# Optimization experiments

Hardware: AMD Instinct MI355X
Metric: run time of the kernel (lower is better)

Reference implementation:

```python
import jax, jax.numpy as jnp
import numpy as np

HEAD_DIM = 128
NUM_HEADS = 16
NUM_KV_HEADS = 16
ROPE_MAX_POS = 4096
ROPE_BASE = 10000.0


def _rope_tables(seq_len):
    # cos/sin cached tables: [S, D/2]
    inv_freq = 1.0 / (ROPE_BASE ** (jnp.arange(0, HEAD_DIM, 2, dtype=jnp.float32) / HEAD_DIM))
    t = jnp.arange(seq_len, dtype=jnp.float32)
    freqs = jnp.outer(t, inv_freq)
    return jnp.cos(freqs), jnp.sin(freqs)


def _apply_rope(x, cos, sin):
    # x: [B, S, H, D]; cos/sin: [S, D/2] -> broadcast over heads as [S, 1, D/2]
    orig_dtype = x.dtype
    c = cos[:, None, :]
    s = sin[:, None, :]
    xf = x.astype(jnp.float32)
    x_real, x_im = jnp.split(xf, 2, axis=-1)  # half-split (not interleaved) RoPE
    x_real_e = x_real * c - x_im * s
    x_im_e = x_im * c + x_real * s
    return jnp.concatenate((x_real_e, x_im_e), axis=-1).astype(orig_dtype)


def setup_inputs() -> dict:
    key = jax.random.key(0)
    k1, k2, k3 = jax.random.split(key, 3)
    B, S, H = 1, 4096, 2048
    hidden_states = jax.random.normal(k1, (B, S, H), dtype=jnp.float32)
    # trunc-normal-ish init, std ~ 1/sqrt(fan_in)
    w_qkv = jax.random.normal(k2, ((NUM_HEADS + 2 * NUM_KV_HEADS) * HEAD_DIM, H), dtype=jnp.float32) / jnp.sqrt(jnp.float32(H))
    w_o = jax.random.normal(k3, (H, NUM_HEADS * HEAD_DIM), dtype=jnp.float32) / jnp.sqrt(jnp.float32(NUM_HEADS * HEAD_DIM))
    return {"hidden_states": hidden_states, "w_qkv": w_qkv, "w_o": w_o}


def reference(hidden_states, w_qkv, w_o):
    B, S, _ = hidden_states.shape
    qkv = jnp.einsum('bsh,oh->bso', hidden_states, w_qkv)
    qkv = qkv.reshape(B, S, NUM_HEADS + 2 * NUM_KV_HEADS, HEAD_DIM)
    q = qkv[:, :, :NUM_HEADS]
    k = qkv[:, :, NUM_HEADS:NUM_HEADS + NUM_KV_HEADS]
    v = qkv[:, :, NUM_HEADS + NUM_KV_HEADS:]

    cos, sin = _rope_tables(S)
    q = _apply_rope(q, cos, sin)
    k = _apply_rope(k, cos, sin)

    scale = 1.0 / jnp.sqrt(jnp.float32(HEAD_DIM)).astype(q.dtype)
    # scores: [B, H, Sq, Sk]
    scores = jnp.einsum('bqhd,bkhd->bhqk', q, k) * scale
    causal = jnp.tril(jnp.ones((S, S), dtype=bool))
    scores = jnp.where(causal[None, None], scores, jnp.finfo(scores.dtype).min)
    probs = jax.nn.softmax(scores, axis=-1)
    attn = jnp.einsum('bhqk,bkhd->bqhd', probs, v)
    attn = attn.reshape(B, S, NUM_HEADS * HEAD_DIM)
    return jnp.einsum('bso,ho->bsh', attn, w_o)
```

## Files before the change

### kernel.cpp

```cpp
#include <hip/hip_runtime.h>

typedef __bf16 bf16;
typedef __bf16 bf16x8 __attribute__((ext_vector_type(8)));
typedef __bf16 bf16x4 __attribute__((ext_vector_type(4)));
typedef float f32x4 __attribute__((ext_vector_type(4)));

#define SEQ 4096
#define QKV_LD 6144
#define HNUM 16

__device__ __forceinline__ void async16(const bf16* g, bf16* l) {
    __builtin_amdgcn_global_load_lds((const __attribute__((address_space(1))) void*)g,
                                     (__attribute__((address_space(3))) void*)l, 16, 0, 0);
}

__global__ __launch_bounds__(256) void prep(const float* __restrict__ X, bf16* __restrict__ Xb,
                                            const float* __restrict__ Wq, bf16* __restrict__ Wqb,
                                            const float* __restrict__ Wo, bf16* __restrict__ Wob,
                                            float* __restrict__ T) {
    const int b = blockIdx.x, t = threadIdx.x;
    if (b < 12288) {
        const float* src;
        bf16* dst;
        int off;
        if (b < 4096)       { src = X;  dst = Xb;  off = b; }
        else if (b < 10240) { src = Wq; dst = Wqb; off = b - 4096; }
        else                { src = Wo; dst = Wob; off = b - 10240; }
        int i = (off * 256 + t) * 8;
        f32x4 a = *(const f32x4*)(src + i);
        f32x4 c = *(const f32x4*)(src + i + 4);
        bf16x8 w;
#pragma unroll
        for (int j = 0; j < 4; j++) { w[j] = (bf16)a[j]; w[4 + j] = (bf16)c[j]; }
        *(bf16x8*)(dst + i) = w;
    } else {
        int i = (b - 12288) * 256 + t;
        int s = i >> 6, d = i & 63;
        float inv_freq = powf(10000.0f, -(float)d * (1.0f / 64.0f));
        float ang = (float)s * inv_freq;
        T[2 * i]     = cosf(ang);
        T[2 * i + 1] = sinf(ang);
    }
}

__device__ __forceinline__ bf16x8 ldfrag(const bf16* slot, int row, int qd) {
    int lin  = row * 64 + qd * 16;
    int phys = lin ^ (((lin >> 9) & 1) << 5);
    return *(const bf16x8*)((const char*)slot + phys);
}

#define STAGE2(SG, SGR0, STT, SKK, SBUF, SMAT)                                  \
    {                                                                           \
        int tcl = (STT) < NT ? (STT) : NT - 1;                                  \
        const bf16* gsrc = (SG) + (size_t)(SGR0)*K + tcl * 64 + (SKK)*32;       \
        bf16* sl = &LDS[SBUF][SMAT][SKK][0];                                    \
        async16(gsrc + g0, (bf16*)((char*)sl + lb0));                           \
        async16(gsrc + g1, (bf16*)((char*)sl + lb1));                           \
    }

#define PHASE(QM, KKI, LOADB, SG, SGR0, STT, SKK, SBUF, SMAT, DOVM)             \
    {                                                                           \
        if (LOADB) {                                                            \
            _Pragma("unroll") for (int j = 0; j < 4; j++)                       \
                bB[j] = ldfrag(&LDS[bi][1][KKI][0],                             \
                               (wc >> 1) * 128 + (wc & 1) * 32 +                \
                                   (j & 1) * 16 + (j >> 1) * 64 + ln, qd);      \
        }                                                                       \
        bf16x8 aA[4];                                                           \
        _Pragma("unroll") for (int i = 0; i < 4; i++)                           \
            aA[i] = ldfrag(&LDS[bi][0][KKI][0],                                 \
                           wr * 128 + (QM)*64 + i * 16 + ln, qd);               \
        STAGE2(SG, SGR0, STT, SKK, SBUF, SMAT);                                 \
        __builtin_amdgcn_sched_barrier(0);                                      \
        if (DOVM) {                                                             \
            asm volatile("s_waitcnt vmcnt(4)" ::: "memory");                    \
            __builtin_amdgcn_sched_barrier(0);                                  \
        }                                                                       \
        __builtin_amdgcn_s_barrier();                                           \
        __builtin_amdgcn_sched_barrier(0);                                      \
        __builtin_amdgcn_s_setprio(1);                                          \
        _Pragma("unroll") for (int i = 0; i < 4; i++)                           \
            _Pragma("unroll") for (int j = 0; j < 4; j++)                       \
                acc[(QM)*4 + i][j] = __builtin_amdgcn_mfma_f32_16x16x32_bf16(   \
                    aA[i], bB[j], acc[(QM)*4 + i][j], 0, 0, 0);                 \
        __builtin_amdgcn_s_setprio(0);                                          \
        __builtin_amdgcn_sched_barrier(0);                                      \
        __builtin_amdgcn_s_barrier();                                           \
        __builtin_amdgcn_sched_barrier(0);                                      \
    }

template <int ROPE>
__global__ __launch_bounds__(512, 2) void gemm256_nt(const bf16* __restrict__ A,
                                                     const bf16* __restrict__ B,
                                                     bf16* __restrict__ C,
                                                     int M, int N, int K,
                                                     const float* __restrict__ T) {
    __shared__ __align__(16) bf16 LDS[2][2][2][256 * 32];
    const int tid  = threadIdx.x;
    const int wave = tid >> 6, lane = tid & 63;
    const int qd = lane >> 4, ln = lane & 15;
    const int wr = wave >> 2, wc = wave & 3;
    const int lin = blockIdx.x + gridDim.x * blockIdx.y;
    const int nwg = gridDim.x * gridDim.y;
    const int job = (lin & 7) * (nwg >> 3) + (lin >> 3);
    const int bm = (job % gridDim.x) * 256;
    const int bn = (job / gridDim.x) * 256;
    const int NT = K >> 6;

    const int seg0 = wave * 2, seg1 = seg0 + 1;
    const int Pr0 = seg0 * 1024 + lane * 16;
    const int Pr1 = seg1 * 1024 + lane * 16;
    const int Lr0 = Pr0 ^ (((Pr0 >> 9) & 1) << 5);
    const int Lr1 = Pr1 ^ (((Pr1 >> 9) & 1) << 5);
    const size_t g0 = (size_t)(Lr0 >> 6) * K + ((Lr0 & 63) >> 1);
    const size_t g1 = (size_t)(Lr1 >> 6) * K + ((Lr1 & 63) >> 1);
    const int lb0 = seg0 * 1024, lb1 = seg1 * 1024;

    f32x4 acc[8][4] = {};

    STAGE2(A, bm, 0, 0, 0, 0);
    STAGE2(B, bn, 0, 0, 0, 1);
    STAGE2(A, bm, 0, 1, 0, 0);
    STAGE2(B, bn, 0, 1, 0, 1);
    STAGE2(A, bm, 1, 0, 1, 0);
    STAGE2(B, bn, 1, 0, 1, 1);
    __builtin_amdgcn_sched_barrier(0);
    asm volatile("s_waitcnt vmcnt(4)" ::: "memory");
    __builtin_amdgcn_sched_barrier(0);
    __builtin_amdgcn_s_barrier();
    __builtin_amdgcn_sched_barrier(0);

    for (int t = 0; t < NT; ++t) {
        const int bi = t & 1;
        bf16x8 bB[4];
        PHASE(0, 0, 1, A, bm, t + 1, 1, bi ^ 1, 0, 0)
        PHASE(1, 0, 0, B, bn, t + 1, 1, bi ^ 1, 1, 0)
        PHASE(0, 1, 1, A, bm, t + 2, 0, bi,     0, 0)
        PHASE(1, 1, 0, B, bn, t + 2, 0, bi,     1, 1)
    }
    asm volatile("s_waitcnt vmcnt(0)" ::: "memory");

    const int colb = bn + (wc >> 1) * 128 + (wc & 1) * 32 + ln;
    if (ROPE && bn < 4096) {
        const float2* T2 = (const float2*)T;
        const int d0 = (wc & 1) * 32 + ln;
#pragma unroll
        for (int mi = 0; mi < 8; mi++)
#pragma unroll
            for (int r = 0; r < 4; r++) {
                int row = bm + wr * 128 + mi * 16 + qd * 4 + r;
                float2 cs0 = T2[(size_t)row * 64 + d0];
                float2 cs1 = T2[(size_t)row * 64 + d0 + 16];
                float a0 = acc[mi][0][r], b0 = acc[mi][2][r];
                float a1 = acc[mi][1][r], b1 = acc[mi][3][r];
                size_t o = (size_t)row * N + colb;
                C[o]      = (bf16)(a0 * cs0.x - b0 * cs0.y);
                C[o + 64] = (bf16)(b0 * cs0.x + a0 * cs0.y);
                C[o + 16] = (bf16)(a1 * cs1.x - b1 * cs1.y);
                C[o + 80] = (bf16)(b1 * cs1.x + a1 * cs1.y);
            }
    } else {
#pragma unroll
        for (int mi = 0; mi < 8; mi++)
#pragma unroll
            for (int r = 0; r < 4; r++) {
                size_t o = (size_t)(bm + wr * 128 + mi * 16 + qd * 4 + r) * N + colb;
                C[o]      = (bf16)acc[mi][0][r];
                C[o + 16] = (bf16)acc[mi][1][r];
                C[o + 64] = (bf16)acc[mi][2][r];
                C[o + 80] = (bf16)acc[mi][3][r];
            }
    }
}

__device__ __forceinline__ bf16x8 ldfragB(const bf16* slot, int row, int qd) {
    int lin  = row * 64 + qd * 16;
    int phys = lin ^ (((lin >> 9) & 1) << 5);
    return *(const bf16x8*)((const char*)slot + phys);
}

#define STG(TT, KKI, BUF)                                                      \
    {                                                                          \
        int tcl = (TT) < NT ? (TT) : NT - 1;                                   \
        const bf16* As = A + (size_t)bm * K + tcl * 64 + (KKI)*32;             \
        const bf16* Bs = B + (size_t)bn * K + tcl * 64 + (KKI)*32;             \
        async16(As + gA,  (bf16*)((char*)&LA[BUF][KKI][0] + lbA));             \
        async16(Bs + gB0, (bf16*)((char*)&LB[BUF][KKI][0] + lbB0));            \
        async16(Bs + gB1, (bf16*)((char*)&LB[BUF][KKI][0] + lbB1));            \
    }

#define PH(KKI, TT, SKK, SBUF, DOVM)                                           \
    {                                                                          \
        bf16x8 aA[4], bB[4];                                                   \
        _Pragma("unroll") for (int i = 0; i < 4; i++)                          \
            aA[i] = ldfragB(&LA[bi][KKI][0], wr * 64 + i * 16 + ln, qd);       \
        _Pragma("unroll") for (int j = 0; j < 4; j++)                          \
            bB[j] = ldfragB(&LB[bi][KKI][0], wc * 64 + j * 16 + ln, qd);       \
        STG(TT, SKK, SBUF);                                                    \
        __builtin_amdgcn_sched_barrier(0);                                     \
        if (DOVM) {                                                            \
            asm volatile("s_waitcnt vmcnt(3)" ::: "memory");                   \
            __builtin_amdgcn_sched_barrier(0);                                 \
        }                                                                      \
        __builtin_amdgcn_s_barrier();                                          \
        __builtin_amdgcn_sched_barrier(0);                                     \
        __builtin_amdgcn_s_setprio(1);                                         \
        _Pragma("unroll") for (int i = 0; i < 4; i++)                          \
            _Pragma("unroll") for (int j = 0; j < 4; j++)                      \
                acc[i][j] = __builtin_amdgcn_mfma_f32_16x16x32_bf16(           \
                    aA[i], bB[j], acc[i][j], 0, 0, 0);                         \
        __builtin_amdgcn_s_setprio(0);                                         \
        __builtin_amdgcn_sched_barrier(0);                                     \
        __builtin_amdgcn_s_barrier();                                          \
        __builtin_amdgcn_sched_barrier(0);                                     \
    }

template <int C_F32>
__global__ __launch_bounds__(512, 2) void gemm128x256(const bf16* __restrict__ A,
                                                      const bf16* __restrict__ B,
                                                      void* __restrict__ Cp,
                                                      int M, int N, int K) {
    __shared__ __align__(16) bf16 LA[2][2][128 * 32];
    __shared__ __align__(16) bf16 LB[2][2][256 * 32];
    const int tid  = threadIdx.x;
    const int wave = tid >> 6, lane = tid & 63;
    const int qd = lane >> 4, ln = lane & 15;
    const int wr = wave >> 2, wc = wave & 3;
    const int lin = blockIdx.x + gridDim.x * blockIdx.y;
    const int nwg = gridDim.x * gridDim.y;
    const int job = (lin & 7) * (nwg >> 3) + (lin >> 3);
    const int bm = (job % gridDim.x) * 128;
    const int bn = (job / gridDim.x) * 256;
    const int NT = K >> 6;

    const int PrA  = wave * 1024 + lane * 16;
    const int PrB0 = (2 * wave) * 1024 + lane * 16;
    const int PrB1 = PrB0 + 1024;
    const int LrA  = PrA  ^ (((PrA  >> 9) & 1) << 5);
    const int LrB0 = PrB0 ^ (((PrB0 >> 9) & 1) << 5);
    const int LrB1 = PrB1 ^ (((PrB1 >> 9) & 1) << 5);
    const size_t gA  = (size_t)(LrA  >> 6) * K + ((LrA  & 63) >> 1);
    const size_t gB0 = (size_t)(LrB0 >> 6) * K + ((LrB0 & 63) >> 1);
    const size_t gB1 = (size_t)(LrB1 >> 6) * K + ((LrB1 & 63) >> 1);
    const int lbA = wave * 1024, lbB0 = 2 * wave * 1024, lbB1 = lbB0 + 1024;

    f32x4 acc[4][4] = {};

    STG(0, 0, 0);
    STG(0, 1, 0);
    STG(1, 0, 1);
    __builtin_amdgcn_sched_barrier(0);
    asm volatile("s_waitcnt vmcnt(3)" ::: "memory");
    __builtin_amdgcn_sched_barrier(0);
    __builtin_amdgcn_s_barrier();
    __builtin_amdgcn_sched_barrier(0);

    for (int t = 0; t < NT; ++t) {
        const int bi = t & 1;
        PH(0, t + 1, 1, bi ^ 1, 0)
        PH(1, t + 2, 0, bi,     1)
    }
    asm volatile("s_waitcnt vmcnt(0)" ::: "memory");

    const size_t cb = (size_t)(bm + wr * 64 + qd * 4) * N + (bn + wc * 64 + ln);
#pragma unroll
    for (int mi = 0; mi < 4; mi++)
#pragma unroll
        for (int j = 0; j < 4; j++)
#pragma unroll
            for (int r = 0; r < 4; r++) {
                size_t idx = cb + (size_t)(mi * 16 + r) * N + j * 16;
                if (C_F32) ((float*)Cp)[idx] = acc[mi][j][r];
                else       ((bf16*)Cp)[idx]  = (bf16)acc[mi][j][r];
            }
}

template <int A_F32, int B_F32, int C_F32>
__global__ __launch_bounds__(256) void gemm_nt(const void* __restrict__ Ap,
                                               const void* __restrict__ Bp,
                                               void* __restrict__ Cp,
                                               int M, int N, int K) {
    __shared__ __align__(16) bf16 sA[128 * 32];
    __shared__ __align__(16) bf16 sB[128 * 32];
    const int tid  = threadIdx.x;
    const int wave = tid >> 6, lane = tid & 63;
    const int qd = lane >> 4, ln = lane & 15;
    const int bm = blockIdx.x * 128, bn = blockIdx.y * 128;
    const int wm = (wave >> 1) * 64, wn = (wave & 1) * 64;

    const int srow = wave * 16 + (lane >> 2);
    const int scol = (lane & 3) * 8;
    const size_t rowoff = (size_t)srow * K + scol;
    const size_t rowskip = (size_t)64 * K;

    const bf16* Ab = (const bf16*)Ap + (size_t)bm * K + rowoff;
    const bf16* Bb = (const bf16*)Bp + (size_t)bn * K + rowoff;
    const float* Af = (const float*)Ap + (size_t)bm * K + rowoff;
    const float* Bf = (const float*)Bp + (size_t)bn * K + rowoff;
    bf16* sAd0 = &sA[(wave * 16) * 32];
    bf16* sAd1 = &sA[(64 + wave * 16) * 32];
    bf16* sBd0 = &sB[(wave * 16) * 32];
    bf16* sBd1 = &sB[(64 + wave * 16) * 32];
    bf16* sAw0 = &sA[srow * 32 + scol];
    bf16* sAw1 = &sA[(64 + srow) * 32 + scol];
    bf16* sBw0 = &sB[srow * 32 + scol];
    bf16* sBw1 = &sB[(64 + srow) * 32 + scol];

    f32x4 acc[4][4] = {};
    for (int k0 = 0; k0 < K; k0 += 32) {
        if (A_F32) {
            f32x4 u0 = *(const f32x4*)(Af + k0);
            f32x4 u1 = *(const f32x4*)(Af + k0 + 4);
            f32x4 u2 = *(const f32x4*)(Af + rowskip + k0);
            f32x4 u3 = *(const f32x4*)(Af + rowskip + k0 + 4);
            bf16x8 w0, w1;
#pragma unroll
            for (int i = 0; i < 4; i++) { w0[i] = (bf16)u0[i]; w0[4 + i] = (bf16)u1[i];
                                          w1[i] = (bf16)u2[i]; w1[4 + i] = (bf16)u3[i]; }
            *(bf16x8*)sAw0 = w0;
            *(bf16x8*)sAw1 = w1;
        } else {
            async16(Ab + k0, sAd0);
            async16(Ab + rowskip + k0, sAd1);
        }
        if (B_F32) {
            f32x4 u0 = *(const f32x4*)(Bf + k0);
            f32x4 u1 = *(const f32x4*)(Bf + k0 + 4);
            f32x4 u2 = *(const f32x4*)(Bf + rowskip + k0);
            f32x4 u3 = *(const f32x4*)(Bf + rowskip + k0 + 4);
            bf16x8 w0, w1;
#pragma unroll
            for (int i = 0; i < 4; i++) { w0[i] = (bf16)u0[i]; w0[4 + i] = (bf16)u1[i];
                                          w1[i] = (bf16)u2[i]; w1[4 + i] = (bf16)u3[i]; }
            *(bf16x8*)sBw0 = w0;
            *(bf16x8*)sBw1 = w1;
        } else {
            async16(Bb + k0, sBd0);
            async16(Bb + rowskip + k0, sBd1);
        }
        __syncthreads();
        bf16x8 af[4], bfr[4];
#pragma unroll
        for (int i = 0; i < 4; i++)
            af[i] = *(const bf16x8*)&sA[(wm + i * 16 + ln) * 32 + qd * 8];
#pragma unroll
        for (int j = 0; j < 4; j++)
            bfr[j] = *(const bf16x8*)&sB[(wn + j * 16 + ln) * 32 + qd * 8];
#pragma unroll
        for (int i = 0; i < 4; i++)
#pragma unroll
            for (int j = 0; j < 4; j++)
                acc[i][j] = __builtin_amdgcn_mfma_f32_16x16x32_bf16(af[i], bfr[j], acc[i][j], 0, 0, 0);
        __syncthreads();
    }
    const size_t cbase = (size_t)(bm + wm + qd * 4) * N + (bn + wn + ln);
#pragma unroll
    for (int i = 0; i < 4; i++)
#pragma unroll
        for (int j = 0; j < 4; j++)
#pragma unroll
            for (int r = 0; r < 4; r++) {
                size_t idx = cbase + (size_t)(i * 16 + r) * N + j * 16;
                if (C_F32) ((float*)Cp)[idx] = acc[i][j][r];
                else       ((bf16*)Cp)[idx] = (bf16)acc[i][j][r];
            }
}

__global__ __launch_bounds__(256) void transpose_v(const bf16* __restrict__ QKV,
                                                   bf16* __restrict__ VT) {
    __shared__ bf16 tl[64][65];
    const int b2 = blockIdx.x;
    const int s0 = (b2 & 63) * 64;
    const int d0 = (b2 >> 6) * 64;
    const int r = threadIdx.x >> 3, c = threadIdx.x & 7;
#pragma unroll
    for (int u = 0; u < 2; u++) {
        bf16x8 v = *(const bf16x8*)(QKV + (size_t)(s0 + u * 32 + r) * QKV_LD + 4096 + d0 + c * 8);
#pragma unroll
        for (int e = 0; e < 8; e++) tl[u * 32 + r][c * 8 + e] = v[e];
    }
    __syncthreads();
#pragma unroll
    for (int u = 0; u < 2; u++) {
        bf16x8 w;
#pragma unroll
        for (int e = 0; e < 8; e++) w[e] = tl[c * 8 + e][u * 32 + r];
        *(bf16x8*)(VT + (size_t)(d0 + u * 32 + r) * SEQ + s0 + c * 8) = w;
    }
}

__global__ __launch_bounds__(256) void rope_k_inline(bf16* __restrict__ QKV) {
    const int s  = blockIdx.x;
    const int t  = threadIdx.x;
    const int hh = (blockIdx.y << 2) + (t >> 6);
    const int d  = t & 63;
    bf16* p = QKV + (size_t)s * QKV_LD + hh * 128 + d;
    float x0 = (float)p[0];
    float x1 = (float)p[64];
    float inv_freq = powf(10000.0f, -(float)d * (1.0f / 64.0f));
    float ang = (float)s * inv_freq;
    float c = cosf(ang), sn = sinf(ang);
    p[0]  = (bf16)(x0 * c - x1 * sn);
    p[64] = (bf16)(x1 * c + x0 * sn);
}

template <int USE_VT>
__global__ __launch_bounds__(256, 2) void flash_attn(const bf16* __restrict__ QKV,
                                                     const bf16* __restrict__ VT,
                                                     bf16* __restrict__ O) {
    __shared__ __align__(16) bf16 sK[64 * 128];
    __shared__ __align__(16) bf16 sV[128 * 64];
    __shared__ __align__(16) bf16 sP[4][32 * 64];
    const int tid  = threadIdx.x;
    const int wave = tid >> 6, lane = tid & 63;
    const int qd = lane >> 4, ln = lane & 15;
    const int h  = blockIdx.x;
    const int y  = blockIdx.y;
    const int qtile = (y < 16) ? (31 - y) : (y - 16);
    const int qw0 = qtile * 128 + wave * 32;
    const int nkv = 2 * qtile + 2;
    const float scale = 0.08838834764831843f;

    bf16x8 Qf[2][4];
#pragma unroll
    for (int qt = 0; qt < 2; qt++) {
        const bf16* Qg = QKV + (size_t)(qw0 + qt * 16 + ln) * QKV_LD + h * 128;
#pragma unroll
        for (int ks = 0; ks < 4; ks++) {
            bf16x8 q8 = *(const bf16x8*)(Qg + ks * 32 + qd * 8);
#pragma unroll
            for (int e = 0; e < 8; e++) q8[e] = (bf16)((float)q8[e] * scale);
            Qf[qt][ks] = q8;
        }
    }

    f32x4 Oacc[2][8] = {};
    float l_i[2] = {0.0f, 0.0f};

    const int krow = tid >> 4;
    const int kblk = tid & 15;
    const int vrow = tid >> 3;
    const int vblk = tid & 7;
    const int vd   = tid & 127;
    const int vh   = tid >> 7;
    const bf16* Kg  = QKV + 2048 + h * 128;
    const bf16* Vg  = QKV + 4096 + h * 128;
    const bf16* VTg = VT + (size_t)h * 128 * SEQ;

    bf16x8 Kpre[4], Vpre[4];
#pragma unroll
    for (int rr = 0; rr < 4; rr++)
        Kpre[rr] = *(const bf16x8*)(Kg + (size_t)(rr * 16 + krow) * QKV_LD + kblk * 8);
    if (USE_VT) {
#pragma unroll
        for (int u = 0; u < 4; u++)
            Vpre[u] = *(const bf16x8*)(VTg + (size_t)(u * 32 + vrow) * SEQ + vblk * 8);
    } else {
#pragma unroll
        for (int u = 0; u < 4; u++)
#pragma unroll
            for (int j = 0; j < 8; j++)
                Vpre[u][j] = Vg[(size_t)(vh * 32 + u * 8 + j) * QKV_LD + vd];
    }

    for (int kt = 0; kt < nkv; kt++) {
        const int kbase = kt * 64;
#pragma unroll
        for (int rr = 0; rr < 4; rr++) {
            int kv = rr * 16 + krow;
            *(bf16x8*)&sK[kv * 128 + ((kblk ^ (kv & 7)) * 8)] = Kpre[rr];
        }
        if (USE_VT) {
#pragma unroll
            for (int u = 0; u < 4; u++) {
                int d = u * 32 + vrow;
                *(bf16x8*)&sV[d * 64 + ((vblk ^ (d & 7)) * 8)] = Vpre[u];
            }
        } else {
#pragma unroll
            for (int u = 0; u < 4; u++)
                *(bf16x8*)&sV[vd * 64 + (((vh * 4 + u) ^ (vd & 7)) * 8)] = Vpre[u];
        }
        __syncthreads();
        if (kt + 1 < nkv) {
            const int nb = kbase + 64;
#pragma unroll
            for (int rr = 0; rr < 4; rr++)
                Kpre[rr] = *(const bf16x8*)(Kg + (size_t)(nb + rr * 16 + krow) * QKV_LD + kblk * 8);
            if (USE_VT) {
#pragma unroll
                for (int u = 0; u < 4; u++)
                    Vpre[u] = *(const bf16x8*)(VTg + (size_t)(u * 32 + vrow) * SEQ + nb + vblk * 8);
            } else {
#pragma unroll
                for (int u = 0; u < 4; u++)
#pragma unroll
                    for (int j = 0; j < 8; j++)
                        Vpre[u][j] = Vg[(size_t)(nb + vh * 32 + u * 8 + j) * QKV_LD + vd];
            }
        }
        if (kbase <= qw0 + 31) {
            f32x4 Sacc[2][4] = {};
            __builtin_amdgcn_s_setprio(1);
#pragma unroll
            for (int ks = 0; ks < 4; ks++)
#pragma unroll
                for (int j = 0; j < 4; j++) {
                    bf16x8 af = *(const bf16x8*)&sK[(j * 16 + ln) * 128 + (((ks * 4 + qd) ^ (ln & 7)) * 8)];
                    Sacc[0][j] = __builtin_amdgcn_mfma_f32_16x16x32_bf16(af, Qf[0][ks], Sacc[0][j], 0, 0, 0);
                    Sacc[1][j] = __builtin_amdgcn_mfma_f32_16x16x32_bf16(af, Qf[1][ks], Sacc[1][j], 0, 0, 0);
                }
            __builtin_amdgcn_s_setprio(0);
#pragma unroll
            for (int qt = 0; qt < 2; qt++) {
                const int qs = qw0 + qt * 16;
                if (kbase + 63 > qs) {
#pragma unroll
                    for (int j = 0; j < 4; j++)
#pragma unroll
                        for (int r = 0; r < 4; r++)
                            if (kbase + j * 16 + qd * 4 + r > qs + ln) Sacc[qt][j][r] = -1e30f;
                }
                float psum = 0.0f;
#pragma unroll
                for (int j = 0; j < 4; j++) {
                    bf16x4 p4;
#pragma unroll
                    for (int r = 0; r < 4; r++) {
                        float p = __expf(Sacc[qt][j][r]);
                        psum += p;
                        p4[r] = (bf16)p;
                    }
                    int blk = (j * 2 + (qd >> 1)) ^ (ln & 7);
                    *(bf16x4*)&sP[wave][(qt * 16 + ln) * 64 + blk * 8 + (qd & 1) * 4] = p4;
                }
                psum += __shfl_xor(psum, 16);
                psum += __shfl_xor(psum, 32);
                l_i[qt] += psum;
            }
            __builtin_amdgcn_s_setprio(1);
#pragma unroll
            for (int ks = 0; ks < 2; ks++) {
                bf16x8 pf0 = *(const bf16x8*)&sP[wave][(0 * 16 + ln) * 64 + (((ks * 4 + qd) ^ (ln & 7)) * 8)];
                bf16x8 pf1 = *(const bf16x8*)&sP[wave][(1 * 16 + ln) * 64 + (((ks * 4 + qd) ^ (ln & 7)) * 8)];
#pragma unroll
                for (int dt = 0; dt < 8; dt++) {
                    bf16x8 vf = *(const bf16x8*)&sV[(dt * 16 + ln) * 64 + (((ks * 4 + qd) ^ (ln & 7)) * 8)];
                    Oacc[0][dt] = __builtin_amdgcn_mfma_f32_16x16x32_bf16(pf0, vf, Oacc[0][dt], 0, 0, 0);
                    Oacc[1][dt] = __builtin_amdgcn_mfma_f32_16x16x32_bf16(pf1, vf, Oacc[1][dt], 0, 0, 0);
                }
            }
            __builtin_amdgcn_s_setprio(0);
        }
        __syncthreads();
    }
#pragma unroll
    for (int qt = 0; qt < 2; qt++) {
        float linv[4];
#pragma unroll
        for (int r = 0; r < 4; r++)
            linv[r] = 1.0f / __shfl(l_i[qt], (lane & 48) | (qd * 4 + r));
        bf16* Ob = O + (size_t)(qw0 + qt * 16 + qd * 4) * 2048 + h * 128 + ln;
#pragma unroll
        for (int dt = 0; dt < 8; dt++)
#pragma unroll
            for (int r = 0; r < 4; r++)
                Ob[(size_t)r * 2048 + dt * 16] = (bf16)(Oacc[qt][dt][r] * linv[r]);
    }
}

extern "C" void kernel_launch(void* const* d_in, const int* in_sizes, int n_in,
                              void* d_out, int out_size, void* d_ws, size_t ws_size,
                              hipStream_t stream) {
    const float* X    = (const float*)d_in[0];
    const float* Wqkv = (const float*)d_in[1];
    const float* Wo   = (const float*)d_in[2];
    float* out = (float*)d_out;
    bf16* QKV = (bf16*)d_ws;
    bf16* ATT = QKV + (size_t)4096 * 6144;

    const size_t nX = (size_t)4096 * 2048, nWq = (size_t)6144 * 2048, nWo = (size_t)2048 * 2048;
    const size_t need = (nX * 3 + nWq * 2 + nWo) * 2 + nX * 2;

    if (ws_size >= need) {
        bf16* Xb  = ATT + nX;
        bf16* Wqb = Xb + nX;
        bf16* Wob = Wqb + nWq;
        bf16*  VT  = Xb;
        float* Tab = (float*)ATT;
        prep<<<13312, 256, 0, stream>>>(X, Xb, Wqkv, Wqb, Wo, Wob, Tab);
        gemm256_nt<1><<<dim3(16, 24), 512, 0, stream>>>(Xb, Wqb, QKV, 4096, 6144, 2048, Tab);
        transpose_v<<<2048, 256, 0, stream>>>(QKV, VT);
        flash_attn<1><<<dim3(HNUM, 32), 256, 0, stream>>>(QKV, VT, ATT);
        gemm128x256<1><<<dim3(32, 8), 512, 0, stream>>>(ATT, Wob, out, 4096, 2048, 2048);
    } else {
        gemm_nt<1, 1, 0><<<dim3(32, 48), 256, 0, stream>>>(X, Wqkv, QKV, 4096, 6144, 2048);
        rope_k_inline<<<dim3(4096, 8), 256, 0, stream>>>(QKV);
        flash_attn<0><<<dim3(HNUM, 32), 256, 0, stream>>>(QKV, (const bf16*)nullptr, ATT);
        gemm_nt<0, 1, 1><<<dim3(32, 16), 256, 0, stream>>>(ATT, Wo, out, 4096, 2048, 2048);
    }
}
```

Before: 417.8 us.

## Fuse V transpose into QKV GEMM epilogue and drop transpose kernel

The QKV GEMM epilogue now writes the V columns transposed, in place inside the QKV buffer's V region, so the separate transpose_v kernel and its extra buffer are removed. flash_attn reads V^T from the same buffer through a remapped row index that splits the sequence into two 2048-element halves per row. It also replaces the swizzled workgroup-to-tile mapping in both GEMMs with plain blockIdx tiling. This saves one launch and a full pass over V, but the epilogue writes 8-byte pieces strided across rows, and removing the swizzle may hurt L2 reuse.

```diff
diff --git a/kernel.cpp b/kernel.cpp
--- a/kernel.cpp
+++ b/kernel.cpp
@@ -100,11 +100,7 @@
     const int wave = tid >> 6, lane = tid & 63;
     const int qd = lane >> 4, ln = lane & 15;
     const int wr = wave >> 2, wc = wave & 3;
-    const int lin = blockIdx.x + gridDim.x * blockIdx.y;
-    const int nwg = gridDim.x * gridDim.y;
-    const int job = (lin & 7) * (nwg >> 3) + (lin >> 3);
-    const int bm = (job % gridDim.x) * 256;
-    const int bn = (job / gridDim.x) * 256;
+    const int bm = blockIdx.x * 256, bn = blockIdx.y * 256;
     const int NT = K >> 6;
 
     const int seg0 = wave * 2, seg1 = seg0 + 1;
@@ -159,6 +155,22 @@
                 C[o + 16] = (bf16)(a1 * cs1.x - b1 * cs1.y);
                 C[o + 80] = (bf16)(b1 * cs1.x + a1 * cs1.y);
             }
+    } else if (ROPE) {
+        bf16* Vb = C + 4096;
+#pragma unroll
+        for (int mi = 0; mi < 8; mi++) {
+            const int row = bm + wr * 128 + mi * 16 + qd * 4;
+            const int rhi = row >> 11;
+            const int rlo = row & 2047;
+#pragma unroll
+            for (int j = 0; j < 4; j++) {
+                const int dh = colb - 4096 + (j & 1) * 16 + (j >> 1) * 64;
+                bf16x4 w;
+#pragma unroll
+                for (int r = 0; r < 4; r++) w[r] = (bf16)acc[mi][j][r];
+                *(bf16x4*)(Vb + (size_t)(2 * dh + rhi) * N + rlo) = w;
+            }
+        }
     } else {
 #pragma unroll
         for (int mi = 0; mi < 8; mi++)
@@ -226,11 +238,7 @@
     const int wave = tid >> 6, lane = tid & 63;
     const int qd = lane >> 4, ln = lane & 15;
     const int wr = wave >> 2, wc = wave & 3;
-    const int lin = blockIdx.x + gridDim.x * blockIdx.y;
-    const int nwg = gridDim.x * gridDim.y;
-    const int job = (lin & 7) * (nwg >> 3) + (lin >> 3);
-    const int bm = (job % gridDim.x) * 128;
-    const int bn = (job / gridDim.x) * 256;
+    const int bm = blockIdx.x * 128, bn = blockIdx.y * 256;
     const int NT = K >> 6;
 
     const int PrA  = wave * 1024 + lane * 16;
@@ -364,29 +372,6 @@
                 if (C_F32) ((float*)Cp)[idx] = acc[i][j][r];
                 else       ((bf16*)Cp)[idx] = (bf16)acc[i][j][r];
             }
-}
-
-__global__ __launch_bounds__(256) void transpose_v(const bf16* __restrict__ QKV,
-                                                   bf16* __restrict__ VT) {
-    __shared__ bf16 tl[64][65];
-    const int b2 = blockIdx.x;
-    const int s0 = (b2 & 63) * 64;
-    const int d0 = (b2 >> 6) * 64;
-    const int r = threadIdx.x >> 3, c = threadIdx.x & 7;
-#pragma unroll
-    for (int u = 0; u < 2; u++) {
-        bf16x8 v = *(const bf16x8*)(QKV + (size_t)(s0 + u * 32 + r) * QKV_LD + 4096 + d0 + c * 8);
-#pragma unroll
-        for (int e = 0; e < 8; e++) tl[u * 32 + r][c * 8 + e] = v[e];
-    }
-    __syncthreads();
-#pragma unroll
-    for (int u = 0; u < 2; u++) {
-        bf16x8 w;
-#pragma unroll
-        for (int e = 0; e < 8; e++) w[e] = tl[c * 8 + e][u * 32 + r];
-        *(bf16x8*)(VT + (size_t)(d0 + u * 32 + r) * SEQ + s0 + c * 8) = w;
-    }
 }
 
 __global__ __launch_bounds__(256) void rope_k_inline(bf16* __restrict__ QKV) {
@@ -406,7 +391,6 @@
 
 template <int USE_VT>
 __global__ __launch_bounds__(256, 2) void flash_attn(const bf16* __restrict__ QKV,
-                                                     const bf16* __restrict__ VT,
                                                      bf16* __restrict__ O) {
     __shared__ __align__(16) bf16 sK[64 * 128];
     __shared__ __align__(16) bf16 sV[128 * 64];
@@ -445,7 +429,7 @@
     const int vh   = tid >> 7;
     const bf16* Kg  = QKV + 2048 + h * 128;
     const bf16* Vg  = QKV + 4096 + h * 128;
-    const bf16* VTg = VT + (size_t)h * 128 * SEQ;
+    const bf16* Vtb = QKV + 4096;
 
     bf16x8 Kpre[4], Vpre[4];
 #pragma unroll
@@ -453,8 +437,10 @@
         Kpre[rr] = *(const bf16x8*)(Kg + (size_t)(rr * 16 + krow) * QKV_LD + kblk * 8);
     if (USE_VT) {
 #pragma unroll
-        for (int u = 0; u < 4; u++)
-            Vpre[u] = *(const bf16x8*)(VTg + (size_t)(u * 32 + vrow) * SEQ + vblk * 8);
+        for (int u = 0; u < 4; u++) {
+            int dh = h * 128 + u * 32 + vrow;
+            Vpre[u] = *(const bf16x8*)(Vtb + (size_t)(2 * dh) * QKV_LD + vblk * 8);
+        }
     } else {
 #pragma unroll
         for (int u = 0; u < 4; u++)
@@ -489,8 +475,11 @@
                 Kpre[rr] = *(const bf16x8*)(Kg + (size_t)(nb + rr * 16 + krow) * QKV_LD + kblk * 8);
             if (USE_VT) {
 #pragma unroll
-                for (int u = 0; u < 4; u++)
-                    Vpre[u] = *(const bf16x8*)(VTg + (size_t)(u * 32 + vrow) * SEQ + nb + vblk * 8);
+                for (int u = 0; u < 4; u++) {
+                    int dh = h * 128 + u * 32 + vrow;
+                    Vpre[u] = *(const bf16x8*)(Vtb + (size_t)(2 * dh + (nb >> 11)) * QKV_LD +
+                                               (nb & 2047) + vblk * 8);
+                }
             } else {
 #pragma unroll
                 for (int u = 0; u < 4; u++)
@@ -586,17 +575,15 @@
         bf16* Xb  = ATT + nX;
         bf16* Wqb = Xb + nX;
         bf16* Wob = Wqb + nWq;
-        bf16*  VT  = Xb;
         float* Tab = (float*)ATT;
         prep<<<13312, 256, 0, stream>>>(X, Xb, Wqkv, Wqb, Wo, Wob, Tab);
         gemm256_nt<1><<<dim3(16, 24), 512, 0, stream>>>(Xb, Wqb, QKV, 4096, 6144, 2048, Tab);
-        transpose_v<<<2048, 256, 0, stream>>>(QKV, VT);
-        flash_attn<1><<<dim3(HNUM, 32), 256, 0, stream>>>(QKV, VT, ATT);
+        flash_attn<1><<<dim3(HNUM, 32), 256, 0, stream>>>(QKV, ATT);
         gemm128x256<1><<<dim3(32, 8), 512, 0, stream>>>(ATT, Wob, out, 4096, 2048, 2048);
     } else {
         gemm_nt<1, 1, 0><<<dim3(32, 48), 256, 0, stream>>>(X, Wqkv, QKV, 4096, 6144, 2048);
         rope_k_inline<<<dim3(4096, 8), 256, 0, stream>>>(QKV);
-        flash_attn<0><<<dim3(HNUM, 32), 256, 0, stream>>>(QKV, (const bf16*)nullptr, ATT);
+        flash_attn<0><<<dim3(HNUM, 32), 256, 0, stream>>>(QKV, ATT);
         gemm_nt<0, 1, 1><<<dim3(32, 16), 256, 0, stream>>>(ATT, Wo, out, 4096, 2048, 2048);
     }
 }
```

Result: faster. 401.0 us (-4.0%).
